# Kernel optimization log

Hardware: AMD Instinct MI355X
Metric: run time of the kernel (lower is better)

Reference implementation:

```python
import jax, jax.numpy as jnp
import numpy as np

B, C, H, W = 16, 64, 256, 256


def setup_inputs() -> dict:
    key = jax.random.key(0)
    k1, k2 = jax.random.split(key)
    x = jax.random.normal(k1, (B, C, H, W), dtype=jnp.float32)
    # theta near identity so the warp samples mostly in-bounds (realistic STN regime)
    ident = jnp.array([1.0, 0.0, 0.0, 0.0, 1.0, 0.0], dtype=jnp.float32)
    theta = ident[None, :] + 0.1 * jax.random.normal(k2, (B, 6), dtype=jnp.float32)
    return {"x": x, "theta": theta}


def _affine_grid(theta, h, w):
    # F.affine_grid with align_corners=False (torch default):
    # normalized pixel centers in [-1+1/W, 1-1/W]
    xs = (jnp.arange(w, dtype=jnp.float32) + 0.5) * (2.0 / w) - 1.0
    ys = (jnp.arange(h, dtype=jnp.float32) + 0.5) * (2.0 / h) - 1.0
    gx, gy = jnp.meshgrid(xs, ys)  # each [H, W], 'xy' indexing
    base = jnp.stack([gx, gy, jnp.ones_like(gx)], axis=-1)  # [H, W, 3]
    # grid[..., 0] = sampled x coord, grid[..., 1] = sampled y coord
    return jnp.einsum('bij,hwj->bhwi', theta.reshape(-1, 2, 3), base)  # [B, H, W, 2]


def _grid_sample_bilinear_zeros(x, grid):
    # F.grid_sample(mode='bilinear', padding_mode='zeros', align_corners=False)
    b, c, h, w = x.shape
    ix = ((grid[..., 0] + 1.0) * w - 1.0) * 0.5  # [B, H, W] source x (pixel units)
    iy = ((grid[..., 1] + 1.0) * h - 1.0) * 0.5  # [B, H, W] source y
    ix0f = jnp.floor(ix)
    iy0f = jnp.floor(iy)
    tx = ix - ix0f  # fractional offsets (differentiable w.r.t. grid)
    ty = iy - iy0f
    ix0 = ix0f.astype(jnp.int32)
    iy0 = iy0f.astype(jnp.int32)
    ix1 = ix0 + 1
    iy1 = iy0 + 1

    def corner(yi, xi, wgt):
        valid = (xi >= 0) & (xi < w) & (yi >= 0) & (yi < h)
        xc = jnp.clip(xi, 0, w - 1)
        yc = jnp.clip(yi, 0, h - 1)
        # per-batch gather: img[:, yy, xx] -> [C, H, W]
        v = jax.vmap(lambda img, yy, xx: img[:, yy, xx])(x, yc, xc)  # [B, C, H, W]
        return v * (wgt * valid.astype(x.dtype))[:, None, :, :]

    out = (corner(iy0, ix0, (1.0 - tx) * (1.0 - ty))
           + corner(iy0, ix1, tx * (1.0 - ty))
           + corner(iy1, ix0, (1.0 - tx) * ty)
           + corner(iy1, ix1, tx * ty))
    return out


def reference(x, theta):
    grid = _affine_grid(theta, x.shape[2], x.shape[3])
    return _grid_sample_bilinear_zeros(x, grid)
```

## Files before the change

kernel.cpp:

```cpp
#include <hip/hip_runtime.h>


constexpr int B = 16, C = 64, H = 256, W = 256;
constexpr int HW = H * W;
constexpr int CHW = C * HW;
constexpr int HB = 4;
constexpr int NBLK = B * (H / HB);

__global__ __launch_bounds__(256) void st_affine_kernel(
    const float* __restrict__ x, const float* __restrict__ theta,
    float* __restrict__ out)
{
    const int bid = blockIdx.x;
    constexpr int CHUNK = NBLK / 8;
    const int wg = (bid & 7) * CHUNK + (bid >> 3);

    const int b  = wg >> 6;
    const int h0 = (wg & 63) * HB;
    const int w  = threadIdx.x;

    const float* th = theta + b * 6;
    const float t0 = th[0], t1 = th[1], t2 = th[2];
    const float t3 = th[3], t4 = th[4], t5 = th[5];

    const float gx = (w + 0.5f) * (2.0f / W) - 1.0f;

    float wt[HB][4];
    int   off[HB][4];
#pragma unroll
    for (int hh = 0; hh < HB; ++hh) {
        const float gy = (h0 + hh + 0.5f) * (2.0f / H) - 1.0f;

        const float sx = t0 * gx + t1 * gy + t2;
        const float sy = t3 * gx + t4 * gy + t5;

        const float ix = ((sx + 1.0f) * (float)W - 1.0f) * 0.5f;
        const float iy = ((sy + 1.0f) * (float)H - 1.0f) * 0.5f;

        const float ix0f = floorf(ix);
        const float iy0f = floorf(iy);
        const float tx = ix - ix0f;
        const float ty = iy - iy0f;
        const int ix0 = (int)ix0f, iy0 = (int)iy0f;
        const int ix1 = ix0 + 1,   iy1 = iy0 + 1;

        const float vx0 = (ix0 >= 0 && ix0 < W) ? 1.0f : 0.0f;
        const float vx1 = (ix1 >= 0 && ix1 < W) ? 1.0f : 0.0f;
        const float vy0 = (iy0 >= 0 && iy0 < H) ? 1.0f : 0.0f;
        const float vy1 = (iy1 >= 0 && iy1 < H) ? 1.0f : 0.0f;

        wt[hh][0] = (1.0f - tx) * (1.0f - ty) * vx0 * vy0;
        wt[hh][1] = tx          * (1.0f - ty) * vx1 * vy0;
        wt[hh][2] = (1.0f - tx) * ty          * vx0 * vy1;
        wt[hh][3] = tx          * ty          * vx1 * vy1;

        const int cx0 = min(max(ix0, 0), W - 1);
        const int cx1 = min(max(ix1, 0), W - 1);
        const int cy0 = min(max(iy0, 0), H - 1);
        const int cy1 = min(max(iy1, 0), H - 1);

        off[hh][0] = cy0 * W + cx0;
        off[hh][1] = cy0 * W + cx1;
        off[hh][2] = cy1 * W + cx0;
        off[hh][3] = cy1 * W + cx1;
    }

    const float* __restrict__ xb = x + (size_t)b * CHW;
    float* __restrict__ ob = out + (size_t)b * CHW + h0 * W + w;

#pragma unroll 2
    for (int c = 0; c < C; ++c) {
        const float* __restrict__ xc = xb + c * HW;
        float* __restrict__ oc = ob + (size_t)c * HW;
#pragma unroll
        for (int hh = 0; hh < HB; ++hh) {
            const float v = xc[off[hh][0]] * wt[hh][0]
                          + xc[off[hh][1]] * wt[hh][1]
                          + xc[off[hh][2]] * wt[hh][2]
                          + xc[off[hh][3]] * wt[hh][3];
            __builtin_nontemporal_store(v, oc + hh * W);
        }
    }
}

extern "C" void kernel_launch(void* const* d_in, const int* in_sizes, int n_in,
                              void* d_out, int out_size, void* d_ws, size_t ws_size,
                              hipStream_t stream) {
    const float* x     = (const float*)d_in[0];
    const float* theta = (const float*)d_in[1];
    float* out = (float*)d_out;

    dim3 grid(NBLK), block(256);
    st_affine_kernel<<<grid, block, 0, stream>>>(x, theta, out);
}
```

Before: 558.7 us.

## Stage source footprint of 64x8 output tiles in LDS per channel

Output tiles are now 64 wide by 8 tall. Each block computes the bounding box of the affine-mapped source region for its tile, cooperatively loads that window into shared memory for each channel, and reads the four bilinear taps from LDS instead of issuing scattered global gathers. A fallback path with direct global gathers handles tiles whose footprint exceeds the LDS capacity. The change adds two __syncthreads per channel and a serialised load-then-compute pattern with no double buffering. It also uses fewer output rows per thread, which may expose more latency.

```diff
diff --git a/kernel.cpp b/kernel.cpp
--- a/kernel.cpp
+++ b/kernel.cpp
@@ -4,38 +4,76 @@
 constexpr int B = 16, C = 64, H = 256, W = 256;
 constexpr int HW = H * W;
 constexpr int CHW = C * HW;
-constexpr int HB = 4;
-constexpr int NBLK = B * (H / HB);
+
+constexpr int WT = 64, HT = 8;
+constexpr int NYT = H / HT;
+constexpr int NXT = W / WT;
+constexpr int NBLK = B * NXT * NYT;
+constexpr int NRCAP = 40;
+constexpr int WSCAP = 108;
 
 __global__ __launch_bounds__(256) void st_affine_kernel(
     const float* __restrict__ x, const float* __restrict__ theta,
     float* __restrict__ out)
 {
+    __shared__ float smem[NRCAP * WSCAP];
+
     const int bid = blockIdx.x;
     constexpr int CHUNK = NBLK / 8;
-    const int wg = (bid & 7) * CHUNK + (bid >> 3);
+    const int swz = (bid & 7) * CHUNK + (bid >> 3);
 
-    const int b  = wg >> 6;
-    const int h0 = (wg & 63) * HB;
-    const int w  = threadIdx.x;
+    const int ht   = swz & (NYT - 1);
+    const int rest = swz >> 5;
+    const int wt   = rest & (NXT - 1);
+    const int b    = rest >> 2;
+    const int h0 = ht * HT, w0 = wt * WT;
+
+    const int tw = threadIdx.x & 63;
+    const int tp = threadIdx.x >> 6;
 
     const float* th = theta + b * 6;
     const float t0 = th[0], t1 = th[1], t2 = th[2];
     const float t3 = th[3], t4 = th[4], t5 = th[5];
 
-    const float gx = (w + 0.5f) * (2.0f / W) - 1.0f;
+    const float gxl = (w0 + 0.5f)          * (2.0f / W) - 1.0f;
+    const float gxr = (w0 + WT - 1 + 0.5f) * (2.0f / W) - 1.0f;
+    const float gyt = (h0 + 0.5f)          * (2.0f / H) - 1.0f;
+    const float gyb = (h0 + HT - 1 + 0.5f) * (2.0f / H) - 1.0f;
 
-    float wt[HB][4];
-    int   off[HB][4];
+    auto mapix = [&](float gx, float gy) {
+        return ((t0 * gx + t1 * gy + t2 + 1.0f) * (float)W - 1.0f) * 0.5f;
+    };
+    auto mapiy = [&](float gx, float gy) {
+        return ((t3 * gx + t4 * gy + t5 + 1.0f) * (float)H - 1.0f) * 0.5f;
+    };
+
+    const float ixa = mapix(gxl, gyt), ixb = mapix(gxr, gyt),
+                ixc = mapix(gxl, gyb), ixd = mapix(gxr, gyb);
+    const float iya = mapiy(gxl, gyt), iyb = mapiy(gxr, gyt),
+                iyc = mapiy(gxl, gyb), iyd = mapiy(gxr, gyb);
+
+    const float ixmin = fminf(fminf(ixa, ixb), fminf(ixc, ixd));
+    const float ixmax = fmaxf(fmaxf(ixa, ixb), fmaxf(ixc, ixd));
+    const float iymin = fminf(fminf(iya, iyb), fminf(iyc, iyd));
+    const float iymax = fmaxf(fmaxf(iya, iyb), fmaxf(iyc, iyd));
+
+    const int c0 = (int)floorf(ixmin) - 1;
+    const int r0 = (int)floorf(iymin) - 1;
+    const int WS = (int)floorf(ixmax) - c0 + 3;
+    const int NR = (int)floorf(iymax) - r0 + 3;
+
+    int   ldsbase[2];
+    float w00[2], w01[2], w10[2], w11[2];
+    int   off00[2], off01[2], off10[2], off11[2];
+
 #pragma unroll
-    for (int hh = 0; hh < HB; ++hh) {
+    for (int p = 0; p < 2; ++p) {
+        const int hh = tp + p * 4;
+        const float gx = (w0 + tw + 0.5f) * (2.0f / W) - 1.0f;
         const float gy = (h0 + hh + 0.5f) * (2.0f / H) - 1.0f;
 
-        const float sx = t0 * gx + t1 * gy + t2;
-        const float sy = t3 * gx + t4 * gy + t5;
-
-        const float ix = ((sx + 1.0f) * (float)W - 1.0f) * 0.5f;
-        const float iy = ((sy + 1.0f) * (float)H - 1.0f) * 0.5f;
+        const float ix = mapix(gx, gy);
+        const float iy = mapiy(gx, gy);
 
         const float ix0f = floorf(ix);
         const float iy0f = floorf(iy);
@@ -49,36 +87,66 @@
         const float vy0 = (iy0 >= 0 && iy0 < H) ? 1.0f : 0.0f;
         const float vy1 = (iy1 >= 0 && iy1 < H) ? 1.0f : 0.0f;
 
-        wt[hh][0] = (1.0f - tx) * (1.0f - ty) * vx0 * vy0;
-        wt[hh][1] = tx          * (1.0f - ty) * vx1 * vy0;
-        wt[hh][2] = (1.0f - tx) * ty          * vx0 * vy1;
-        wt[hh][3] = tx          * ty          * vx1 * vy1;
+        w00[p] = (1.0f - tx) * (1.0f - ty) * vx0 * vy0;
+        w01[p] = tx          * (1.0f - ty) * vx1 * vy0;
+        w10[p] = (1.0f - tx) * ty          * vx0 * vy1;
+        w11[p] = tx          * ty          * vx1 * vy1;
+
+        const int sxs = min(max(ix0 - c0, 0), WSCAP - 2);
+        const int sys = min(max(iy0 - r0, 0), NRCAP - 2);
+        ldsbase[p] = sys * WSCAP + sxs;
 
         const int cx0 = min(max(ix0, 0), W - 1);
         const int cx1 = min(max(ix1, 0), W - 1);
         const int cy0 = min(max(iy0, 0), H - 1);
         const int cy1 = min(max(iy1, 0), H - 1);
-
-        off[hh][0] = cy0 * W + cx0;
-        off[hh][1] = cy0 * W + cx1;
-        off[hh][2] = cy1 * W + cx0;
-        off[hh][3] = cy1 * W + cx1;
+        off00[p] = cy0 * W + cx0;  off01[p] = cy0 * W + cx1;
+        off10[p] = cy1 * W + cx0;  off11[p] = cy1 * W + cx1;
     }
 
     const float* __restrict__ xb = x + (size_t)b * CHW;
-    float* __restrict__ ob = out + (size_t)b * CHW + h0 * W + w;
+    float* __restrict__ ob = out + (size_t)b * CHW + (size_t)h0 * W + w0 + tw;
 
-#pragma unroll 2
+    if (NR > NRCAP || WS > WSCAP) {
+        for (int c = 0; c < C; ++c) {
+            const float* __restrict__ xc = xb + (size_t)c * HW;
+            float* __restrict__ oc = ob + (size_t)c * HW;
+#pragma unroll
+            for (int p = 0; p < 2; ++p) {
+                const float v = xc[off00[p]] * w00[p] + xc[off01[p]] * w01[p]
+                              + xc[off10[p]] * w10[p] + xc[off11[p]] * w11[p];
+                __builtin_nontemporal_store(v, oc + (tp + p * 4) * W);
+            }
+        }
+        return;
+    }
+
     for (int c = 0; c < C; ++c) {
-        const float* __restrict__ xc = xb + c * HW;
+        const float* __restrict__ xc = xb + (size_t)c * HW;
         float* __restrict__ oc = ob + (size_t)c * HW;
+
+        if (c) __syncthreads();
+        for (int k = tp; k < NR; k += 4) {
+            const int rs = min(max(r0 + k, 0), H - 1);
+            const float* __restrict__ rowp = xc + (rs << 8);
+            float* __restrict__ dst = smem + k * WSCAP;
+            for (int j = tw; j < WS; j += 64) {
+                const int cs = min(max(c0 + j, 0), W - 1);
+                dst[j] = rowp[cs];
+            }
+        }
+        __syncthreads();
+
 #pragma unroll
-        for (int hh = 0; hh < HB; ++hh) {
-            const float v = xc[off[hh][0]] * wt[hh][0]
-                          + xc[off[hh][1]] * wt[hh][1]
-                          + xc[off[hh][2]] * wt[hh][2]
-                          + xc[off[hh][3]] * wt[hh][3];
-            __builtin_nontemporal_store(v, oc + hh * W);
+        for (int p = 0; p < 2; ++p) {
+            const int bse = ldsbase[p];
+            const float a0 = smem[bse];
+            const float a1 = smem[bse + 1];
+            const float a2 = smem[bse + WSCAP];
+            const float a3 = smem[bse + WSCAP + 1];
+            const float v = a0 * w00[p] + a1 * w01[p]
+                          + a2 * w10[p] + a3 * w11[p];
+            __builtin_nontemporal_store(v, oc + (tp + p * 4) * W);
         }
     }
 }
```

Result: slower. 889.5 us (+59.2%).
